# Kernel tuning notes

Hardware: AMD Instinct MI355X
Metric: run time of the kernel (lower is better)

The kernel has to match this reference:

```python
import jax, jax.numpy as jnp
import numpy as np

DIM = 1024
HEADS = 16
HEAD_DIM = DIM // HEADS
RANK = 16
ALPHA = 8.0
SCALING = ALPHA / RANK  # 0.5
SCALE = HEAD_DIM ** (-0.5)
B_, L_ = 2, 2048


def _proj_params(key, std=0.02):
    kW, kb, kA, kB = jax.random.split(key, 4)
    W = jax.random.normal(kW, (DIM, DIM), jnp.float32) * std   # [out, in]
    b = jax.random.normal(kb, (DIM,), jnp.float32) * std
    A = jax.random.normal(kA, (DIM, RANK), jnp.float32) * std  # [out, r]
    Bm = jax.random.normal(kB, (RANK, DIM), jnp.float32) * std # [r, in]
    return W, b, A, Bm


def setup_inputs() -> dict:
    key = jax.random.key(0)
    ks = jax.random.split(key, 6)
    x = jax.random.normal(ks[0], (B_, L_, DIM), jnp.float32)
    attn_bias = jax.random.normal(ks[1], (1, HEADS, L_, L_), jnp.float32) * 0.1
    inp = {"x": x, "attn_bias": attn_bias}
    for name, k in zip("qkvo", ks[2:6]):
        W, b, A, Bm = _proj_params(k)
        inp[f"W{name}"] = W
        inp[f"b{name}"] = b
        inp[f"A{name}"] = A
        inp[f"B{name}"] = Bm
    return inp


def _lora_linear(x, W, b, A, Bm):
    # y = x W^T + b + scaling * ((x @ A) @ B)   (matches torch LoRALinear)
    return x @ W.T + b + SCALING * ((x @ A) @ Bm)


def _split(x):
    B, L, D = x.shape
    return jnp.swapaxes(x.reshape(B, L, HEADS, HEAD_DIM), 1, 2)  # [B,H,L,hd]


def reference(x, attn_bias, Wq, bq, Aq, Bq, Wk, bk, Ak, Bk, Wv, bv, Av, Bv, Wo, bo, Ao, Bo):
    B, L, D = x.shape
    q = _split(_lora_linear(x, Wq, bq, Aq, Bq))
    k = _split(_lora_linear(x, Wk, bk, Ak, Bk))
    v = _split(_lora_linear(x, Wv, bv, Av, Bv))
    scores = jnp.einsum('bhld,bhmd->bhlm', q, k) * SCALE + attn_bias
    attn = jax.nn.softmax(scores, axis=-1)  # dropout p=0 -> identity
    out = jnp.einsum('bhlm,bhmd->bhld', attn, v)
    out = jnp.swapaxes(out, 1, 2).reshape(B, L, D)  # merge heads
    return _lora_linear(out, Wo, bo, Ao, Bo)
```

## Files before the change

kernel.cpp:

```cpp
#include <hip/hip_runtime.h>
#include <cstdint>

typedef __bf16 bf16;
typedef __bf16 bf16x8 __attribute__((ext_vector_type(8)));
typedef __bf16 bf16x4 __attribute__((ext_vector_type(4)));
typedef float  f32x4  __attribute__((ext_vector_type(4)));
typedef float  f32x16 __attribute__((ext_vector_type(16)));
typedef int    i32x4  __attribute__((ext_vector_type(4)));

#define DIM   1024
#define LSEQ  2048
#define NH    16
#define HD    64
#define NTOK  4096

#define AS1C(p) ((const __attribute__((address_space(1))) void*)(unsigned long long)(uintptr_t)(p))
#define AS3P(p) ((__attribute__((address_space(3))) void*)(unsigned int)(uintptr_t)(p))
#define SB0 __builtin_amdgcn_sched_barrier(0)

__device__ __forceinline__ f32x4 mfma16(bf16x8 a, bf16x8 b, f32x4 c) {
  return __builtin_amdgcn_mfma_f32_16x16x32_bf16(a, b, c, 0, 0, 0);
}
__device__ __forceinline__ f32x16 mfma32(bf16x8 a, bf16x8 b, f32x16 c) {
  return __builtin_amdgcn_mfma_f32_32x32x16_bf16(a, b, c, 0, 0, 0);
}
__device__ __forceinline__ int pk2(float a, float b) {
  unsigned short ua = __builtin_bit_cast(unsigned short, (bf16)a);
  unsigned short ub = __builtin_bit_cast(unsigned short, (bf16)b);
  return (int)ua | ((int)ub << 16);
}

__global__ __launch_bounds__(256) void k_cvt(const float* __restrict__ x,
                                             bf16* __restrict__ xb) {
  const int i = (blockIdx.x * 256 + threadIdx.x) * 4;
  const f32x4 v = *(const f32x4*)(x + i);
  bf16x4 o;
  o[0] = (bf16)v[0]; o[1] = (bf16)v[1]; o[2] = (bf16)v[2]; o[3] = (bf16)v[3];
  *(bf16x4*)(xb + i) = o;
}

struct WeffArgs {
  const float* W[4]; const float* A[4]; const float* B[4]; bf16* out[4];
};

__global__ __launch_bounds__(256) void k_weff(WeffArgs args) {
  const int o = blockIdx.x;
  const int z = blockIdx.y;
  const float* __restrict__ W  = args.W[z];
  const float* __restrict__ A  = args.A[z];
  const float* __restrict__ Bm = args.B[z];
  bf16* __restrict__ out = args.out[z];
  float Bo[16];
#pragma unroll
  for (int r = 0; r < 16; ++r) Bo[r] = Bm[r * DIM + o];
#pragma unroll
  for (int j = 0; j < 4; ++j) {
    const int d = j * 256 + (int)threadIdx.x;
    const float* Ar = A + (size_t)d * 16;
    float acc = 0.f;
#pragma unroll
    for (int r = 0; r < 16; ++r) acc += Ar[r] * Bo[r];
    out[(size_t)o * DIM + d] = (bf16)(W[(size_t)o * DIM + d] + 0.5f * acc);
  }
}

template <int NF, bool F32OUT>
__device__ __forceinline__ void gemm_body(const bf16* __restrict__ X,
                                          const bf16* __restrict__ W,
                                          const float* __restrict__ bias,
                                          void* __restrict__ out,
                                          float scale, int m0, int n0) {
  constexpr int BN = NF * 32;
  __shared__ __align__(16) bf16 As[128 * 32];
  __shared__ __align__(16) bf16 Bs[BN * 32];
  const int tid  = threadIdx.x;
  const int lane = tid & 63, w = tid >> 6;
  const int l15 = lane & 15, l4 = lane >> 4;
  const int wr = w >> 1, wc = w & 1;
  const int srow = w * 16 + (lane >> 2);
  const int scol = (lane & 3) * 8;

  f32x4 acc[4][NF] = {};
  const bf16* ag = X + (size_t)m0 * DIM;
  const bf16* bg = W + (size_t)n0 * DIM;

  for (int kt = 0; kt < DIM / 32; ++kt) {
    const int k0 = kt * 32;
#pragma unroll
    for (int j = 0; j < 2; ++j) {
      const int row = j * 64 + srow;
      __builtin_amdgcn_global_load_lds(AS1C(ag + (size_t)row * DIM + k0 + scol),
                                       AS3P(As + (j * 64 + w * 16) * 32), 16, 0, 0);
      if (j * 64 < BN)
        __builtin_amdgcn_global_load_lds(AS1C(bg + (size_t)row * DIM + k0 + scol),
                                         AS3P(Bs + (j * 64 + w * 16) * 32), 16, 0, 0);
    }
    __syncthreads();
    bf16x8 af[4], bfr[NF];
#pragma unroll
    for (int m = 0; m < 4; ++m)
      af[m] = *(const bf16x8*)(As + (wr * 64 + m * 16 + l15) * 32 + l4 * 8);
#pragma unroll
    for (int n = 0; n < NF; ++n)
      bfr[n] = *(const bf16x8*)(Bs + (wc * NF * 16 + n * 16 + l15) * 32 + l4 * 8);
#pragma unroll
    for (int m = 0; m < 4; ++m)
#pragma unroll
      for (int n = 0; n < NF; ++n)
        acc[m][n] = mfma16(af[m], bfr[n], acc[m][n]);
    __syncthreads();
  }

#pragma unroll
  for (int m = 0; m < 4; ++m) {
    const int r0 = m0 + wr * 64 + m * 16 + l4 * 4;
#pragma unroll
    for (int n = 0; n < NF; ++n) {
      const int c = n0 + wc * NF * 16 + n * 16 + l15;
      const float bc = bias[c];
#pragma unroll
      for (int t = 0; t < 4; ++t) {
        const float y = (acc[m][n][t] + bc) * scale;
        if constexpr (F32OUT)
          ((float*)out)[(size_t)(r0 + t) * DIM + c] = y;
        else
          ((bf16*)out)[(size_t)(r0 + t) * DIM + c] = (bf16)y;
      }
    }
  }
}

__global__ __launch_bounds__(256) void k_gemm_qkv(
    const bf16* __restrict__ xb, const bf16* __restrict__ weff,
    const float* __restrict__ bq, const float* __restrict__ bk,
    const float* __restrict__ bv,
    bf16* __restrict__ q, bf16* __restrict__ k, bf16* __restrict__ v) {
  const int z = blockIdx.z;
  const bf16* W = weff + (size_t)z * DIM * DIM;
  const float* bias = (z == 0) ? bq : (z == 1) ? bk : bv;
  bf16* out = (z == 0) ? q : (z == 1) ? k : v;
  const float scale = (z == 0) ? 0.125f : 1.0f;
  gemm_body<4, false>(xb, W, bias, out, scale, blockIdx.x * 128, blockIdx.y * 128);
}

__global__ __launch_bounds__(256) void k_gemm_o(
    const bf16* __restrict__ ctx, const bf16* __restrict__ weffo,
    const float* __restrict__ bo, float* __restrict__ out) {
  gemm_body<2, true>(ctx, weffo, bo, out, 1.0f, blockIdx.x * 128, blockIdx.y * 64);
}

__global__ __launch_bounds__(256) void k_vfrag(const bf16* __restrict__ v,
                                               const bf16* __restrict__ k,
                                               bf16* __restrict__ vf,
                                               bf16* __restrict__ kf) {
  const int lt = blockIdx.x, bh = blockIdx.y;
  const int b = bh >> 4, h = bh & 15;
  __shared__ __align__(16) bf16 tile[64][72];
  const int tid = threadIdx.x;
  const int r = tid >> 2, c0 = (tid & 3) * 16;
  const bf16* src = v + (size_t)(b * LSEQ + lt * 64) * DIM + h * HD;
  *(bf16x8*)(&tile[r][c0])     = *(const bf16x8*)(src + (size_t)r * DIM + c0);
  *(bf16x8*)(&tile[r][c0 + 8]) = *(const bf16x8*)(src + (size_t)r * DIM + c0 + 8);
  __syncthreads();
  const int w = tid >> 6, lane = tid & 63, l31 = lane & 31, hi = lane >> 5;
  {
    const int tt = w >> 1, n = w & 1;
    const int t = lt * 2 + tt;
#pragma unroll
    for (int c = 0; c < 2; ++c) {
      bf16 tmp[8];
#pragma unroll
      for (int j = 0; j < 8; ++j)
        tmp[j] = tile[tt * 32 + c * 16 + hi * 8 + j][n * 32 + l31];
      *(bf16x8*)(vf + ((((size_t)bh * 64 + t) * 4 + n * 2 + c) * 64 + lane) * 8) =
          *(bf16x8*)tmp;
    }
  }
  {
    const int t = lt * 2 + (w & 1);
    const bf16* krow = k + (size_t)(b * LSEQ + t * 32 + l31) * DIM + h * HD + hi * 8;
#pragma unroll
    for (int cc = 0; cc < 2; ++cc) {
      const int c = (w >> 1) + cc * 2;
      *(bf16x8*)(kf + ((((size_t)bh * 64 + t) * 4 + c) * 64 + lane) * 8) =
          *(const bf16x8*)(krow + c * 16);
    }
  }
}

__global__ __launch_bounds__(256, 2) void k_attn(
    const bf16* __restrict__ q, const bf16* __restrict__ kf,
    const bf16* __restrict__ vf, const float* __restrict__ bias,
    bf16* __restrict__ ctx) {
  const int tid = threadIdx.x, w = tid >> 6, lane = tid & 63;
  const int l31 = lane & 31, hi = lane >> 5;
  const int bb = w >> 1, qh = w & 1;
  const int h = blockIdx.x & 15;
  const int q0 = (blockIdx.x >> 4) * 64;

  __shared__ __align__(16) bf16  kls[2][3][2048];
  __shared__ __align__(16) bf16  vls[2][3][2048];
  __shared__ __align__(16) float bls[2][3][1024];

  const bf16* qrow = q + (size_t)(bb * LSEQ + q0 + qh * 32 + l31) * DIM + h * HD;
  bf16x8 Qf[4];
#pragma unroll
  for (int c = 0; c < 4; ++c) Qf[c] = *(const bf16x8*)(qrow + c * 16 + hi * 8);

  const int part2  = qh * 2;
  const int bpart2 = bb * 2;
  const int lr = lane >> 3, lc = lane & 7;
  const bf16* ksrc = kf + (size_t)(bb * NH + h) * 64 * 2048 + part2 * 512 + lane * 8;
  const bf16* vsrc = vf + (size_t)(bb * NH + h) * 64 * 2048 + part2 * 512 + lane * 8;
  const float* bsrc =
      bias + ((size_t)h * LSEQ + q0 + qh * 32 + bpart2 * 8 + lr) * LSEQ + 4 * (lc ^ lr);

  f32x16 acc0 = {}, acc1 = {};
  float mrun = -3e38f, lrun = 0.f;

#define STAGE(t_, s_)                                                          \
  {                                                                            \
    __builtin_amdgcn_global_load_lds(AS1C(ksrc + (size_t)(t_) * 2048),         \
                                     AS3P(&kls[bb][s_][part2 * 512]), 16, 0, 0);\
    __builtin_amdgcn_global_load_lds(AS1C(ksrc + (size_t)(t_) * 2048 + 512),   \
                                     AS3P(&kls[bb][s_][part2 * 512 + 512]), 16, 0, 0);\
    __builtin_amdgcn_global_load_lds(AS1C(vsrc + (size_t)(t_) * 2048),         \
                                     AS3P(&vls[bb][s_][part2 * 512]), 16, 0, 0);\
    __builtin_amdgcn_global_load_lds(AS1C(vsrc + (size_t)(t_) * 2048 + 512),   \
                                     AS3P(&vls[bb][s_][part2 * 512 + 512]), 16, 0, 0);\
    __builtin_amdgcn_global_load_lds(AS1C(bsrc + (size_t)(t_) * 32),           \
                                     AS3P(&bls[qh][s_][bpart2 * 256]), 16, 0, 0);\
    __builtin_amdgcn_global_load_lds(AS1C(bsrc + (size_t)(t_) * 32 + 8 * LSEQ),\
                                     AS3P(&bls[qh][s_][bpart2 * 256 + 256]), 16, 0, 0);\
  }

  STAGE(0, 0); SB0;
  STAGE(1, 1); SB0;

  const int sw = (l31 & 7) << 2;
  int sl = 0, ss = 2;
  for (int t = 0; t < 64; ++t) {
    const int tn = (t + 2 > 63) ? 63 : t + 2;
    STAGE(tn, ss); SB0;
    asm volatile("s_waitcnt vmcnt(12)" ::: "memory");
    __builtin_amdgcn_s_barrier();

    bf16x8 Kf[4], Vf[2][2];
    f32x4 br[4];
#pragma unroll
    for (int c = 0; c < 4; ++c)
      Kf[c] = *(const bf16x8*)(&kls[bb][sl][c * 512 + lane * 8]);
#pragma unroll
    for (int u = 0; u < 4; ++u)
      Vf[u >> 1][u & 1] = *(const bf16x8*)(&vls[bb][sl][u * 512 + lane * 8]);
#pragma unroll
    for (int g = 0; g < 4; ++g)
      br[g] = *(const f32x4*)(
          &bls[qh][sl][l31 * 32 + (((g << 3) | (hi << 2)) ^ sw)]);
    asm volatile("s_waitcnt lgkmcnt(0)" ::: "memory");
    SB0;
    __builtin_amdgcn_s_barrier();

    f32x16 s = {};
#pragma unroll
    for (int c = 0; c < 4; ++c) s = mfma32(Kf[c], Qf[c], s);
    float p[16];
#pragma unroll
    for (int r = 0; r < 16; ++r) p[r] = s[r] + br[r >> 2][r & 3];
    float m8[8];
#pragma unroll
    for (int i = 0; i < 8; ++i) m8[i] = fmaxf(p[i], p[i + 8]);
    float tm = fmaxf(fmaxf(fmaxf(m8[0], m8[4]), fmaxf(m8[1], m8[5])),
                     fmaxf(fmaxf(m8[2], m8[6]), fmaxf(m8[3], m8[7])));
    tm = fmaxf(tm, __shfl_xor(tm, 32));
    if (!__all(tm <= mrun + 8.0f)) {
      const float mn = fmaxf(mrun, tm);
      const float scl = __expf(mrun - mn);
      mrun = mn;
      lrun *= scl;
#pragma unroll
      for (int r = 0; r < 16; ++r) { acc0[r] *= scl; acc1[r] *= scl; }
    }
#pragma unroll
    for (int r = 0; r < 16; ++r) p[r] = __expf(p[r] - mrun);
    float s8[8];
#pragma unroll
    for (int i = 0; i < 8; ++i) s8[i] = p[i] + p[i + 8];
    float rs = ((s8[0] + s8[1]) + (s8[2] + s8[3])) + ((s8[4] + s8[5]) + (s8[6] + s8[7]));
    rs += __shfl_xor(rs, 32);
    lrun += rs;
#pragma unroll
    for (int c = 0; c < 2; ++c) {
      const int c8 = c * 8;
      const int A0 = pk2(p[c8 + 0], p[c8 + 1]);
      const int A1 = pk2(p[c8 + 2], p[c8 + 3]);
      const int B0 = pk2(p[c8 + 4], p[c8 + 5]);
      const int B1 = pk2(p[c8 + 6], p[c8 + 7]);
      const int pA0 = __shfl_xor(A0, 32), pA1 = __shfl_xor(A1, 32);
      const int pB0 = __shfl_xor(B0, 32), pB1 = __shfl_xor(B1, 32);
      i32x4 fi;
      fi[0] = hi ? pB0 : A0;
      fi[1] = hi ? pB1 : A1;
      fi[2] = hi ? B0 : pA0;
      fi[3] = hi ? B1 : pA1;
      const bf16x8 pf = __builtin_bit_cast(bf16x8, fi);
      acc0 = mfma32(Vf[0][c], pf, acc0);
      acc1 = mfma32(Vf[1][c], pf, acc1);
    }
    sl = (sl == 2) ? 0 : sl + 1;
    ss = (ss == 2) ? 0 : ss + 1;
  }
#undef STAGE

  const float inv = 1.0f / lrun;
  bf16* cp = ctx + (size_t)(bb * LSEQ + q0 + qh * 32 + l31) * DIM + h * HD;
#pragma unroll
  for (int r = 0; r < 16; ++r) {
    const int dr = (r & 3) + 8 * (r >> 2) + 4 * hi;
    cp[dr]      = (bf16)(acc0[r] * inv);
    cp[32 + dr] = (bf16)(acc1[r] * inv);
  }
}

extern "C" void kernel_launch(void* const* d_in, const int* in_sizes, int n_in,
                              void* d_out, int out_size, void* d_ws, size_t ws_size,
                              hipStream_t stream) {
  const float* x  = (const float*)d_in[0];
  const float* ab = (const float*)d_in[1];
  const float* Wq = (const float*)d_in[2];  const float* bq = (const float*)d_in[3];
  const float* Aq = (const float*)d_in[4];  const float* Bq = (const float*)d_in[5];
  const float* Wk = (const float*)d_in[6];  const float* bk = (const float*)d_in[7];
  const float* Ak = (const float*)d_in[8];  const float* Bk = (const float*)d_in[9];
  const float* Wv = (const float*)d_in[10]; const float* bv = (const float*)d_in[11];
  const float* Av = (const float*)d_in[12]; const float* Bv = (const float*)d_in[13];
  const float* Wo = (const float*)d_in[14]; const float* bo = (const float*)d_in[15];
  const float* Ao = (const float*)d_in[16]; const float* Bo = (const float*)d_in[17];

  uint8_t* ws = (uint8_t*)d_ws;
  const size_t SZ = (size_t)NTOK * DIM * sizeof(bf16);
  bf16* xb   = (bf16*)(ws + 0 * SZ);
  bf16* weff = (bf16*)(ws + 1 * SZ);
  bf16* qb   = (bf16*)(ws + 2 * SZ);
  bf16* kb   = (bf16*)(ws + 3 * SZ);
  bf16* vb   = (bf16*)(ws + 4 * SZ);
  bf16* kfb  = (bf16*)(ws + 5 * SZ);
  bf16* vfb  = (bf16*)(ws + 6 * SZ);
  bf16* ctx  = (bf16*)(ws + 7 * SZ);

  k_cvt<<<dim3(NTOK * DIM / 1024), 256, 0, stream>>>(x, xb);

  WeffArgs wa;
  wa.W[0] = Wq; wa.A[0] = Aq; wa.B[0] = Bq; wa.out[0] = weff;
  wa.W[1] = Wk; wa.A[1] = Ak; wa.B[1] = Bk; wa.out[1] = weff + (size_t)DIM * DIM;
  wa.W[2] = Wv; wa.A[2] = Av; wa.B[2] = Bv; wa.out[2] = weff + 2 * (size_t)DIM * DIM;
  wa.W[3] = Wo; wa.A[3] = Ao; wa.B[3] = Bo; wa.out[3] = weff + 3 * (size_t)DIM * DIM;
  k_weff<<<dim3(DIM, 4), 256, 0, stream>>>(wa);

  k_gemm_qkv<<<dim3(32, 8, 3), 256, 0, stream>>>(xb, weff, bq, bk, bv, qb, kb, vb);
  k_vfrag<<<dim3(32, 32), 256, 0, stream>>>(vb, kb, vfb, kfb);
  k_attn<<<dim3(512), 256, 0, stream>>>(qb, kfb, vfb, ab, ctx);
  k_gemm_o<<<dim3(32, 16), 256, 0, stream>>>(ctx, weff + 3 * (size_t)DIM * DIM, bo,
                                             (float*)d_out);
}
```

Baseline: 183.2 us.

## Double attention query tile per block to halve K/V staging per query

The attention kernel now uses 512-thread blocks that each cover 128 queries (four 32-row query slices per batch) instead of 64, with half as many blocks. K/V tiles staged into LDS are shared by twice as many waves, so global K/V traffic per query is halved. Bias staging is reorganised into a single 128-row buffer, and the load distribution and vmcnt wait are adjusted to match. The cost is fewer blocks (256) for the machine, larger LDS use per block, and heavier barriers across 8 waves.

```diff
diff --git a/kernel.cpp b/kernel.cpp
--- a/kernel.cpp
+++ b/kernel.cpp
@@ -188,61 +188,63 @@
   }
 }
 
-__global__ __launch_bounds__(256, 2) void k_attn(
+__global__ __launch_bounds__(512, 2) void k_attn(
     const bf16* __restrict__ q, const bf16* __restrict__ kf,
     const bf16* __restrict__ vf, const float* __restrict__ bias,
     bf16* __restrict__ ctx) {
   const int tid = threadIdx.x, w = tid >> 6, lane = tid & 63;
   const int l31 = lane & 31, hi = lane >> 5;
-  const int bb = w >> 1, qh = w & 1;
+  const int bb = w >> 2, qs = w & 3;
   const int h = blockIdx.x & 15;
-  const int q0 = (blockIdx.x >> 4) * 64;
+  const int q0 = (blockIdx.x >> 4) * 128;
 
   __shared__ __align__(16) bf16  kls[2][3][2048];
   __shared__ __align__(16) bf16  vls[2][3][2048];
-  __shared__ __align__(16) float bls[2][3][1024];
-
-  const bf16* qrow = q + (size_t)(bb * LSEQ + q0 + qh * 32 + l31) * DIM + h * HD;
+  __shared__ __align__(16) float bls[3][4096];
+
+  const bf16* qrow = q + (size_t)(bb * LSEQ + q0 + qs * 32 + l31) * DIM + h * HD;
   bf16x8 Qf[4];
 #pragma unroll
   for (int c = 0; c < 4; ++c) Qf[c] = *(const bf16x8*)(qrow + c * 16 + hi * 8);
 
-  const int part2  = qh * 2;
-  const int bpart2 = bb * 2;
+  const int kvA = 2 * w, kvB = 2 * w + 1;
+  const int kbA = kvA >> 3, vvA = (kvA >> 2) & 1, cA = kvA & 3;
+  const int kbB = kvB >> 3, vvB = (kvB >> 2) & 1, cB = kvB & 3;
+  const bf16* srcA = (vvA ? vf : kf) + (size_t)(kbA * NH + h) * 64 * 2048 + cA * 512 + lane * 8;
+  const bf16* srcB = (vvB ? vf : kf) + (size_t)(kbB * NH + h) * 64 * 2048 + cB * 512 + lane * 8;
+  bf16* dstA = (vvA ? &vls[kbA][0][0] : &kls[kbA][0][0]) + cA * 512 + lane * 8;
+  bf16* dstB = (vvB ? &vls[kbB][0][0] : &kls[kbB][0][0]) + cB * 512 + lane * 8;
   const int lr = lane >> 3, lc = lane & 7;
-  const bf16* ksrc = kf + (size_t)(bb * NH + h) * 64 * 2048 + part2 * 512 + lane * 8;
-  const bf16* vsrc = vf + (size_t)(bb * NH + h) * 64 * 2048 + part2 * 512 + lane * 8;
-  const float* bsrc =
-      bias + ((size_t)h * LSEQ + q0 + qh * 32 + bpart2 * 8 + lr) * LSEQ + 4 * (lc ^ lr);
+  const float* bsA = bias + ((size_t)h * LSEQ + q0 + 16 * w + lr) * LSEQ + 4 * (lc ^ lr);
+  const float* bsB = bsA + (size_t)8 * LSEQ;
+  float* bdA = &bls[0][0] + (2 * w) * 256 + lane * 4;
+  float* bdB = bdA + 256;
 
   f32x16 acc0 = {}, acc1 = {};
   float mrun = -3e38f, lrun = 0.f;
 
 #define STAGE(t_, s_)                                                          \
   {                                                                            \
-    __builtin_amdgcn_global_load_lds(AS1C(ksrc + (size_t)(t_) * 2048),         \
-                                     AS3P(&kls[bb][s_][part2 * 512]), 16, 0, 0);\
-    __builtin_amdgcn_global_load_lds(AS1C(ksrc + (size_t)(t_) * 2048 + 512),   \
-                                     AS3P(&kls[bb][s_][part2 * 512 + 512]), 16, 0, 0);\
-    __builtin_amdgcn_global_load_lds(AS1C(vsrc + (size_t)(t_) * 2048),         \
-                                     AS3P(&vls[bb][s_][part2 * 512]), 16, 0, 0);\
-    __builtin_amdgcn_global_load_lds(AS1C(vsrc + (size_t)(t_) * 2048 + 512),   \
-                                     AS3P(&vls[bb][s_][part2 * 512 + 512]), 16, 0, 0);\
-    __builtin_amdgcn_global_load_lds(AS1C(bsrc + (size_t)(t_) * 32),           \
-                                     AS3P(&bls[qh][s_][bpart2 * 256]), 16, 0, 0);\
-    __builtin_amdgcn_global_load_lds(AS1C(bsrc + (size_t)(t_) * 32 + 8 * LSEQ),\
-                                     AS3P(&bls[qh][s_][bpart2 * 256 + 256]), 16, 0, 0);\
+    __builtin_amdgcn_global_load_lds(AS1C(srcA + (size_t)(t_) * 2048),         \
+                                     AS3P(dstA + (s_) * 2048), 16, 0, 0);      \
+    __builtin_amdgcn_global_load_lds(AS1C(srcB + (size_t)(t_) * 2048),         \
+                                     AS3P(dstB + (s_) * 2048), 16, 0, 0);      \
+    __builtin_amdgcn_global_load_lds(AS1C(bsA + (size_t)(t_) * 32),            \
+                                     AS3P(bdA + (s_) * 4096), 16, 0, 0);       \
+    __builtin_amdgcn_global_load_lds(AS1C(bsB + (size_t)(t_) * 32),            \
+                                     AS3P(bdB + (s_) * 4096), 16, 0, 0);       \
   }
 
   STAGE(0, 0); SB0;
   STAGE(1, 1); SB0;
 
+  const int rr = qs * 32 + l31;
   const int sw = (l31 & 7) << 2;
   int sl = 0, ss = 2;
   for (int t = 0; t < 64; ++t) {
     const int tn = (t + 2 > 63) ? 63 : t + 2;
     STAGE(tn, ss); SB0;
-    asm volatile("s_waitcnt vmcnt(12)" ::: "memory");
+    asm volatile("s_waitcnt vmcnt(8)" ::: "memory");
     __builtin_amdgcn_s_barrier();
 
     bf16x8 Kf[4], Vf[2][2];
@@ -256,7 +258,7 @@
 #pragma unroll
     for (int g = 0; g < 4; ++g)
       br[g] = *(const f32x4*)(
-          &bls[qh][sl][l31 * 32 + (((g << 3) | (hi << 2)) ^ sw)]);
+          &bls[sl][rr * 32 + (((g << 3) | (hi << 2)) ^ sw)]);
     asm volatile("s_waitcnt lgkmcnt(0)" ::: "memory");
     SB0;
     __builtin_amdgcn_s_barrier();
@@ -313,7 +315,7 @@
 #undef STAGE
 
   const float inv = 1.0f / lrun;
-  bf16* cp = ctx + (size_t)(bb * LSEQ + q0 + qh * 32 + l31) * DIM + h * HD;
+  bf16* cp = ctx + (size_t)(bb * LSEQ + q0 + qs * 32 + l31) * DIM + h * HD;
 #pragma unroll
   for (int r = 0; r < 16; ++r) {
     const int dr = (r & 3) + 8 * (r >> 2) + 4 * hi;
@@ -358,7 +360,7 @@
 
   k_gemm_qkv<<<dim3(32, 8, 3), 256, 0, stream>>>(xb, weff, bq, bk, bv, qb, kb, vb);
   k_vfrag<<<dim3(32, 32), 256, 0, stream>>>(vb, kb, vfb, kfb);
-  k_attn<<<dim3(512), 256, 0, stream>>>(qb, kfb, vfb, ab, ctx);
+  k_attn<<<dim3(256), 512, 0, stream>>>(qb, kfb, vfb, ab, ctx);
   k_gemm_o<<<dim3(32, 16), 256, 0, stream>>>(ctx, weff + 3 * (size_t)DIM * DIM, bo,
                                              (float*)d_out);
 }
```

After: 172.1 us. 1.06x faster.
